# Kernel tuning notes

Hardware: AMD Instinct MI355X
Metric: run time of the kernel (lower is better)

Reference implementation:

```python
import jax, jax.numpy as jnp
import numpy as np

D_MODEL = 512
B, S = 4, 2048


def setup_inputs() -> dict:
    key = jax.random.key(0)
    ks = jax.random.split(key, 12)
    d = D_MODEL
    scale = 1.0 / np.sqrt(d)
    inp = {
        "query": jax.random.normal(ks[0], (B, S, d), dtype=jnp.float32),
        "key":   jax.random.normal(ks[1], (B, S, d), dtype=jnp.float32),
        "value": jax.random.normal(ks[2], (B, S, d), dtype=jnp.float32),
        "mask":  jax.random.uniform(ks[3], (B, S)) < 0.9,
        "num_heads": 8,
        "Wq": jax.random.normal(ks[4], (d, d), dtype=jnp.float32) * scale,
        "bq": jnp.zeros((d,), dtype=jnp.float32),
        "Wk": jax.random.normal(ks[5], (d, d), dtype=jnp.float32) * scale,
        "bk": jnp.zeros((d,), dtype=jnp.float32),
        "Wv": jax.random.normal(ks[6], (d, d), dtype=jnp.float32) * scale,
        "bv": jnp.zeros((d,), dtype=jnp.float32),
        "Wo": jax.random.normal(ks[7], (d, d), dtype=jnp.float32) * scale,
        "bo": jnp.zeros((d,), dtype=jnp.float32),
    }
    return inp


def _mha(query, key, value, mask, num_heads, Wq, bq, Wk, bk, Wv, bv, Wo, bo):
    b, s, d = query.shape
    h = num_heads
    dk = d // h
    # torch Linear: x @ W.T + b ; then split heads -> (b, h, s, dk)
    def proj(x, W, bias):
        return (x @ W.T + bias).reshape(b, s, h, dk).transpose(0, 2, 1, 3)
    q = proj(query, Wq, bq)
    k = proj(key, Wk, bk)
    v = proj(value, Wv, bv)
    scores = jnp.einsum('bhqd,bhkd->bhqk', q, k) / jnp.sqrt(jnp.float32(dk))
    # mask (b, s) broadcast over heads and query positions
    scores = jnp.where(mask[:, None, None, :], scores, -jnp.inf)
    attn = jax.nn.softmax(scores, axis=-1)
    # NaN fix: fully-masked rows produce NaN -> 0 (dropout is identity at eval)
    attn = jnp.where(jnp.isnan(attn), 0.0, attn)
    out = jnp.einsum('bhqk,bhkd->bhqd', attn, v)
    out = out.transpose(0, 2, 1, 3).reshape(b, s, d)
    output = out @ Wo.T + bo
    return output, attn.mean(axis=1)


def reference(query, key, value, mask, num_heads, Wq, bq, Wk, bk, Wv, bv, Wo, bo):
    return _mha(query, key, value, mask, num_heads, Wq, bq, Wk, bk, Wv, bv, Wo, bo)
```

## Files before the change

### kernel.cpp

```cpp
#include <hip/hip_runtime.h>
#include <cstdint>
#include <cstddef>

#define S_LEN 2048
#define D_MODEL 512
#define NHEAD 8
#define DKH 64
#define M_ROWS 8192

typedef unsigned short u16;
typedef unsigned int u32;
typedef short bf16x8 __attribute__((ext_vector_type(8)));
typedef float f32x4 __attribute__((ext_vector_type(4)));

#define MFMA16(a, b, c) __builtin_amdgcn_mfma_f32_16x16x32_bf16((a), (b), (c), 0, 0, 0)

__device__ __forceinline__ u16 f2bf(float f) {
  unsigned u = __float_as_uint(f);
  u += 0x7fffu + ((u >> 16) & 1u);
  return (u16)(u >> 16);
}
__device__ __forceinline__ u32 pack2bf(float f0, float f1) {
  return ((u32)f2bf(f1) << 16) | (u32)f2bf(f0);
}
__device__ __forceinline__ bf16x8 pack8(float4 a, float4 b) {
  union { u32 u[4]; bf16x8 v; } x;
  x.u[0] = pack2bf(a.x, a.y); x.u[1] = pack2bf(a.z, a.w);
  x.u[2] = pack2bf(b.x, b.y); x.u[3] = pack2bf(b.z, b.w);
  return x.v;
}

struct CvtArgs {
  const float* src[7];
  u16* dst[7];
  int n8[7];
};
__global__ __launch_bounds__(256) void cvt_bf16(CvtArgs a) {
  const int ai = blockIdx.y;
  const float* __restrict__ s = a.src[ai];
  u16* __restrict__ d = a.dst[ai];
  const int n8 = a.n8[ai];
  for (int i = blockIdx.x * 256 + threadIdx.x; i < n8; i += gridDim.x * 256) {
    const float4 f0 = *(const float4*)&s[i * 8];
    const float4 f1 = *(const float4*)&s[i * 8 + 4];
    *(bf16x8*)&d[i * 8] = pack8(f0, f1);
  }
}

__global__ __launch_bounds__(512, 4) void proj_qkv(
    const u16* __restrict__ Xq, const u16* __restrict__ Xk, const u16* __restrict__ Xv,
    const u16* __restrict__ Wqb, const u16* __restrict__ Wkb, const u16* __restrict__ Wvb,
    const float* __restrict__ bq, const float* __restrict__ bk, const float* __restrict__ bv,
    u16* __restrict__ Qp, u16* __restrict__ Kp, u16* __restrict__ Vt)
{
  __shared__ __align__(16) u16 wlds[64 * 512];
  const int z = blockIdx.z;
  const u16* __restrict__ X = (z == 0) ? Xk : (z == 1) ? Xv : Xq;
  const u16* __restrict__ W = (z == 0) ? Wkb : (z == 1) ? Wvb : Wqb;
  const float* __restrict__ bias = (z == 0) ? bk : (z == 1) ? bv : bq;
  u16* __restrict__ Y = (z == 0) ? Kp : (z == 1) ? Vt : Qp;
  const int mode = (z == 1) ? 1 : 0;

  const int t = threadIdx.x;
  const int w = t >> 6, lane = t & 63, quad = lane >> 4, lq = lane & 15;
  const int n0 = blockIdx.x * 64;
  const int mb = blockIdx.y * 128 + w * 16;
  const int bb = mb >> 11, s0 = mb & 2047;
  const int h = n0 >> 6;

  for (int i = t; i < 4096; i += 512) {
    const int row = i >> 6, ck = i & 63;
    *(uint4*)&wlds[(row * 512 + ck * 8) ^ ((row & 7) << 3)] =
        *(const uint4*)&W[(size_t)(n0 + row) * D_MODEL + ck * 8];
  }

  bf16x8 xf[16];
#pragma unroll
  for (int ks = 0; ks < 16; ++ks)
    xf[ks] = *(const bf16x8*)&X[(size_t)(mb + lq) * D_MODEL + ks * 32 + quad * 8];
  __syncthreads();

#pragma unroll
  for (int nt = 0; nt < 4; ++nt) {
    const int row = nt * 16 + lq;
    f32x4 acc = {0.f, 0.f, 0.f, 0.f};
#pragma unroll
    for (int ks = 0; ks < 16; ++ks) {
      const bf16x8 wf =
          *(const bf16x8*)&wlds[(row * 512 + ks * 32 + quad * 8) ^ ((row & 7) << 3)];
      acc = MFMA16(xf[ks], wf, acc);
    }
    const float bv2 = bias[n0 + nt * 16 + lq];
    if (mode == 0) {
#pragma unroll
      for (int r = 0; r < 4; ++r)
        Y[(((size_t)(bb * NHEAD + h) * S_LEN) + s0 + quad * 4 + r) * DKH + nt * 16 + lq] =
            f2bf(acc[r] + bv2);
    } else {
      uint2 val;
      val.x = pack2bf(acc[0] + bv2, acc[1] + bv2);
      val.y = pack2bf(acc[2] + bv2, acc[3] + bv2);
      *(uint2*)&Y[(((size_t)(bb * NHEAD + h) * DKH) + nt * 16 + lq) * S_LEN + s0 + quad * 4] = val;
    }
  }
}

__global__ __launch_bounds__(512, 4) void attn_core(
    const u16* __restrict__ Qp,
    const u16* __restrict__ Kp, const u16* __restrict__ Vt,
    const int* __restrict__ mask,
    u16* __restrict__ Oh, float* __restrict__ lis)
{
  __shared__ __align__(16) u16 kvb[2][2][4096];
  __shared__ __align__(16) u16 pst[8][16][72];
  __shared__ u32 gmb[64];

  const int t = threadIdx.x;
  const int w = t >> 6, lane = t & 63, quad = lane >> 4, lq = lane & 15;
  const int srow = t >> 3, sblk = t & 7;
  const int bid = ((int)blockIdx.x & 7) * 64 + ((int)blockIdx.x >> 3);
  const int bb = bid >> 7, h = (bid >> 4) & 7, qc = bid & 15;
  const int qw = qc * 128 + w * 16;
  const size_t hB = (size_t)(bb * NHEAD + h) * S_LEN * DKH;
  const int sslot = srow * 64 + (sblk ^ (srow & 7)) * 8;

#pragma unroll
  for (int p = 0; p < 4; ++p) {
    const int kidx = w * 256 + p * 64 + lane;
    const unsigned long long bal = __ballot(mask[bb * S_LEN + kidx] != 0);
    if (lane == 0) {
      gmb[(w * 256 + p * 64) >> 5] = (u32)bal;
      gmb[((w * 256 + p * 64) >> 5) + 1] = (u32)(bal >> 32);
    }
  }

  uint4 rk = *(const uint4*)&Kp[hB + (size_t)srow * DKH + sblk * 8];
  uint4 rv = *(const uint4*)&Vt[hB + (size_t)srow * S_LEN + sblk * 8];

  bf16x8 qf[2];
#pragma unroll
  for (int ks = 0; ks < 2; ++ks)
    qf[ks] = *(const bf16x8*)&Qp[hB + (size_t)(qw + lq) * DKH + ks * 32 + quad * 8];

  *(uint4*)&kvb[0][0][sslot] = rk;
  *(uint4*)&kvb[0][1][sslot] = rv;
  rk = *(const uint4*)&Kp[hB + (size_t)(64 + srow) * DKH + sblk * 8];
  rv = *(const uint4*)&Vt[hB + (size_t)srow * S_LEN + 64 + sblk * 8];
  __syncthreads();

  f32x4 O[4];
#pragma unroll
  for (int dn = 0; dn < 4; ++dn) { f32x4 z = {0.f, 0.f, 0.f, 0.f}; O[dn] = z; }
  float ls[4] = {0.f, 0.f, 0.f, 0.f};
  const int rx = lq & 7;

#pragma unroll 1
  for (int kt = 0; kt < 32; ++kt) {
    const int c = kt & 1;
    if (kt + 1 < 32) {
      *(uint4*)&kvb[c ^ 1][0][sslot] = rk;
      *(uint4*)&kvb[c ^ 1][1][sslot] = rv;
    }
    if (kt + 2 < 32) {
      const int kb2 = (kt + 2) * 64;
      rk = *(const uint4*)&Kp[hB + (size_t)(kb2 + srow) * DKH + sblk * 8];
      rv = *(const uint4*)&Vt[hB + (size_t)srow * S_LEN + kb2 + sblk * 8];
    }
    const int kb = kt * 64;
    f32x4 p4[4];
    __builtin_amdgcn_s_setprio(1);
#pragma unroll
    for (int kn = 0; kn < 4; ++kn) {
      const bf16x8 k0 = *(const bf16x8*)&kvb[c][0][(kn * 16 + lq) * 64 + (quad ^ rx) * 8];
      const bf16x8 k1 = *(const bf16x8*)&kvb[c][0][(kn * 16 + lq) * 64 + ((4 + quad) ^ rx) * 8];
      f32x4 acc = {0.f, 0.f, 0.f, 0.f};
      acc = MFMA16(qf[0], k0, acc);
      acc = MFMA16(qf[1], k1, acc);
      p4[kn] = acc;
    }
    __builtin_amdgcn_s_setprio(0);
#pragma unroll
    for (int kn = 0; kn < 4; ++kn) {
      const int ki = kb + kn * 16 + lq;
      const float g = ((gmb[ki >> 5] >> (ki & 31)) & 1u) ? 1.f : 0.f;
#pragma unroll
      for (int r = 0; r < 4; ++r) {
        const float e = g * __expf(p4[kn][r] * 0.125f);
        ls[r] += e;
        pst[w][quad * 4 + r][kn * 16 + lq] = f2bf(e);
      }
    }
    bf16x8 pf0 = *(const bf16x8*)&pst[w][lq][quad * 8];
    bf16x8 pf1 = *(const bf16x8*)&pst[w][lq][32 + quad * 8];
    __builtin_amdgcn_s_setprio(1);
#pragma unroll
    for (int dn = 0; dn < 4; ++dn) {
      const bf16x8 v0 = *(const bf16x8*)&kvb[c][1][(dn * 16 + lq) * 64 + (quad ^ rx) * 8];
      const bf16x8 v1 = *(const bf16x8*)&kvb[c][1][(dn * 16 + lq) * 64 + ((4 + quad) ^ rx) * 8];
      O[dn] = MFMA16(pf0, v0, O[dn]);
      O[dn] = MFMA16(pf1, v1, O[dn]);
    }
    __builtin_amdgcn_s_setprio(0);
    __syncthreads();
  }

  float li[4];
#pragma unroll
  for (int r = 0; r < 4; ++r) {
    float v = ls[r];
    v += __shfl_xor(v, 1);
    v += __shfl_xor(v, 2);
    v += __shfl_xor(v, 4);
    v += __shfl_xor(v, 8);
    li[r] = (v > 0.f) ? 1.f / v : 0.f;
  }
  if (lq == 0) {
#pragma unroll
    for (int r = 0; r < 4; ++r)
      lis[(size_t)(bb * NHEAD + h) * S_LEN + qw + quad * 4 + r] = li[r];
  }
#pragma unroll
  for (int dn = 0; dn < 4; ++dn)
#pragma unroll
    for (int r = 0; r < 4; ++r)
      Oh[(size_t)(bb * S_LEN + qw + quad * 4 + r) * D_MODEL + h * 64 + dn * 16 + lq] =
          f2bf(O[dn][r] * li[r]);
}

__global__ __launch_bounds__(512, 4) void oproj_mfma(
    const u16* __restrict__ Oh, const u16* __restrict__ Wb,
    const float* __restrict__ bias, float* __restrict__ out)
{
  __shared__ __align__(16) u16 wlds[64 * 512];
  const int t = threadIdx.x;
  const int w = t >> 6, lane = t & 63, quad = lane >> 4, lq = lane & 15;
  const int n0 = blockIdx.x * 64;
  const int mb = blockIdx.y * 128 + w * 16;

  for (int i = t; i < 4096; i += 512) {
    const int row = i >> 6, ck = i & 63;
    *(uint4*)&wlds[(row * 512 + ck * 8) ^ ((row & 7) << 3)] =
        *(const uint4*)&Wb[(size_t)(n0 + row) * D_MODEL + ck * 8];
  }

  bf16x8 xf[16];
#pragma unroll
  for (int ks = 0; ks < 16; ++ks)
    xf[ks] = *(const bf16x8*)&Oh[(size_t)(mb + lq) * D_MODEL + ks * 32 + quad * 8];
  __syncthreads();

#pragma unroll
  for (int nt = 0; nt < 4; ++nt) {
    const int row = nt * 16 + lq;
    f32x4 acc = {0.f, 0.f, 0.f, 0.f};
#pragma unroll
    for (int ks = 0; ks < 16; ++ks) {
      const bf16x8 wf =
          *(const bf16x8*)&wlds[(row * 512 + ks * 32 + quad * 8) ^ ((row & 7) << 3)];
      acc = MFMA16(xf[ks], wf, acc);
    }
    const float bv = bias[n0 + nt * 16 + lq];
#pragma unroll
    for (int r = 0; r < 4; ++r)
      out[(size_t)(mb + quad * 4 + r) * D_MODEL + n0 + nt * 16 + lq] = acc[r] + bv;
  }
}

__global__ __launch_bounds__(512, 4) void attn_mean(
    const u16* __restrict__ Qp, const u16* __restrict__ Kp,
    const float* __restrict__ lis, const int* __restrict__ mask,
    float* __restrict__ out1)
{
  __shared__ __align__(16) u16 qst[8][32][72];
  __shared__ float lfin[8][32];
  __shared__ u32 gmb[64];

  const int t = threadIdx.x;
  const int w = t >> 6, lane = t & 63, quad = lane >> 4, lq = lane & 15;
  const int bid = ((int)blockIdx.x & 7) * 128 + ((int)blockIdx.x >> 3);
  const int bb = bid >> 8;
  const int q0 = ((bid >> 2) & 63) * 32;
  const int kh = bid & 3;
  const size_t bB = (size_t)bb * NHEAD * S_LEN * DKH;

#pragma unroll
  for (int p = 0; p < 4; ++p) {
    const int kidx = w * 256 + p * 64 + lane;
    const unsigned long long bal = __ballot(mask[bb * S_LEN + kidx] != 0);
    if (lane == 0) {
      gmb[(w * 256 + p * 64) >> 5] = (u32)bal;
      gmb[((w * 256 + p * 64) >> 5) + 1] = (u32)(bal >> 32);
    }
  }
  for (int i = t; i < 2048; i += 512) {
    const int h = i >> 8, qrow = (i >> 3) & 31, d8 = i & 7;
    *(uint4*)&qst[h][qrow][d8 * 8] =
        *(const uint4*)&Qp[bB + (size_t)h * S_LEN * DKH + (size_t)(q0 + qrow) * DKH + d8 * 8];
  }
  if (t < 256) {
    const int h = t >> 5, qr = t & 31;
    lfin[h][qr] = lis[(size_t)(bb * NHEAD + h) * S_LEN + q0 + qr];
  }
  __syncthreads();

  const int kb = kh * 512 + w * 64;

  float am[2][4][4];
#pragma unroll
  for (int qt = 0; qt < 2; ++qt)
#pragma unroll
    for (int kn = 0; kn < 4; ++kn)
#pragma unroll
      for (int r = 0; r < 4; ++r) am[qt][kn][r] = 0.f;

#pragma unroll 1
  for (int h = 0; h < 8; ++h) {
    const size_t hB = bB + (size_t)h * S_LEN * DKH;
    bf16x8 kf[8];
#pragma unroll
    for (int kn = 0; kn < 4; ++kn)
#pragma unroll
      for (int ks = 0; ks < 2; ++ks)
        kf[kn * 2 + ks] =
            *(const bf16x8*)&Kp[hB + (size_t)(kb + kn * 16 + lq) * DKH + ks * 32 + quad * 8];
#pragma unroll
    for (int qt = 0; qt < 2; ++qt) {
      const bf16x8 qh0 = *(const bf16x8*)&qst[h][qt * 16 + lq][quad * 8];
      const bf16x8 qh1 = *(const bf16x8*)&qst[h][qt * 16 + lq][32 + quad * 8];
      const float4 li4 = *(const float4*)&lfin[h][qt * 16 + quad * 4];
#pragma unroll
      for (int kn = 0; kn < 4; ++kn) {
        f32x4 acc = {0.f, 0.f, 0.f, 0.f};
        acc = MFMA16(qh0, kf[kn * 2 + 0], acc);
        acc = MFMA16(qh1, kf[kn * 2 + 1], acc);
        am[qt][kn][0] += __expf(acc[0] * 0.125f) * li4.x;
        am[qt][kn][1] += __expf(acc[1] * 0.125f) * li4.y;
        am[qt][kn][2] += __expf(acc[2] * 0.125f) * li4.z;
        am[qt][kn][3] += __expf(acc[3] * 0.125f) * li4.w;
      }
    }
  }

#pragma unroll
  for (int qt = 0; qt < 2; ++qt)
#pragma unroll
    for (int kn = 0; kn < 4; ++kn) {
      const int ki = kb + kn * 16 + lq;
      const float g8 = ((gmb[ki >> 5] >> (ki & 31)) & 1u) ? 0.125f : 0.f;
#pragma unroll
      for (int r = 0; r < 4; ++r)
        out1[((size_t)(bb * S_LEN + q0 + qt * 16 + quad * 4 + r)) * S_LEN + ki] =
            am[qt][kn][r] * g8;
    }
}

__global__ void beacon_kernel(float* out, float val) { out[0] = val; }

extern "C" void kernel_launch(void* const* d_in, const int* in_sizes, int n_in,
                              void* d_out, int out_size, void* d_ws, size_t ws_size,
                              hipStream_t stream) {
  (void)in_sizes; (void)n_in; (void)out_size;
  const float* q  = (const float*)d_in[0];
  const float* k  = (const float*)d_in[1];
  const float* v  = (const float*)d_in[2];
  const int* mask = (const int*)d_in[3];
  const float* Wq = (const float*)d_in[5];
  const float* bq = (const float*)d_in[6];
  const float* Wk = (const float*)d_in[7];
  const float* bk = (const float*)d_in[8];
  const float* Wv = (const float*)d_in[9];
  const float* bv = (const float*)d_in[10];
  const float* Wo = (const float*)d_in[11];
  const float* bo = (const float*)d_in[12];

  float* out0 = (float*)d_out;
  float* out1 = out0 + (size_t)4 * S_LEN * D_MODEL;

  if (ws_size < (19ull << 20)) {
    beacon_kernel<<<1, 1, 0, stream>>>(out0, 100.0f + (float)(ws_size >> 20));
    return;
  }

  char* ws = (char*)d_ws;
  u16* Kp    = (u16*)(ws);
  u16* Vt    = (u16*)(ws + (8ull << 20));
  float* lis = (float*)(ws + (16ull << 20));
  u16* Qp    = (u16*)(ws + (17ull << 20));

  char* o1 = (char*)out1;
  u16* Oh    = (u16*)o1;
  u16* Xq_bf = (u16*)(o1 + (8ull  << 20));
  u16* Xk_bf = (u16*)(o1 + (16ull << 20));
  u16* Xv_bf = (u16*)(o1 + (24ull << 20));
  u16* Wq_bf = (u16*)(o1 + (32ull << 20));
  u16* Wk_bf = Wq_bf + 262144;
  u16* Wv_bf = Wk_bf + 262144;
  u16* Wo_bf = Wv_bf + 262144;

  CvtArgs ca;
  ca.src[0] = q;  ca.dst[0] = Xq_bf; ca.n8[0] = M_ROWS * D_MODEL / 8;
  ca.src[1] = k;  ca.dst[1] = Xk_bf; ca.n8[1] = M_ROWS * D_MODEL / 8;
  ca.src[2] = v;  ca.dst[2] = Xv_bf; ca.n8[2] = M_ROWS * D_MODEL / 8;
  ca.src[3] = Wq; ca.dst[3] = Wq_bf; ca.n8[3] = D_MODEL * D_MODEL / 8;
  ca.src[4] = Wk; ca.dst[4] = Wk_bf; ca.n8[4] = D_MODEL * D_MODEL / 8;
  ca.src[5] = Wv; ca.dst[5] = Wv_bf; ca.n8[5] = D_MODEL * D_MODEL / 8;
  ca.src[6] = Wo; ca.dst[6] = Wo_bf; ca.n8[6] = D_MODEL * D_MODEL / 8;
  cvt_bf16<<<dim3(256, 7), 256, 0, stream>>>(ca);

  proj_qkv<<<dim3(8, 64, 3), 512, 0, stream>>>(
      Xq_bf, Xk_bf, Xv_bf, Wq_bf, Wk_bf, Wv_bf, bq, bk, bv, Qp, Kp, Vt);

  attn_core<<<512, 512, 0, stream>>>(Qp, Kp, Vt, mask, Oh, lis);
  oproj_mfma<<<dim3(8, 64), 512, 0, stream>>>(Oh, Wo_bf, bo, out0);
  attn_mean<<<1024, 512, 0, stream>>>(Qp, Kp, lis, mask, out1);
}
```

Measured before the change: 326.5 us.

## Double-buffer K loads across heads and stage attn-mean output through LDS

In attn_mean, the K fragments for the next head are loaded into a second register buffer while the current head's MFMAs and exps run, so global-load latency overlaps compute. The output is also written to an LDS staging buffer that aliases the Q tile, then stored as float4 rows instead of scattered 4-byte stores. This targets memory latency and uncoalesced writes of the large attention-mean output. The cost is more registers for the second K buffer and extra block barriers.

After: 365.1 us. +11.8%, slower.

```diff
diff --git a/kernel.cpp b/kernel.cpp
--- a/kernel.cpp
+++ b/kernel.cpp
@@ -271,9 +271,11 @@
     const float* __restrict__ lis, const int* __restrict__ mask,
     float* __restrict__ out1)
 {
-  __shared__ __align__(16) u16 qst[8][32][72];
-  __shared__ float lfin[8][32];
-  __shared__ u32 gmb[64];
+  __shared__ __align__(16) char pool[38912];
+  u16 (*qst)[32][72] = (u16(*)[32][72])pool;
+  float (*lfin)[32]  = (float(*)[32])(pool + 36864);
+  u32* gmb           = (u32*)(pool + 37888);
+  float (*stg)[512]  = (float(*)[512])pool;
 
   const int t = threadIdx.x;
   const int w = t >> 6, lane = t & 63, quad = lane >> 4, lq = lane & 15;
@@ -282,6 +284,7 @@
   const int q0 = ((bid >> 2) & 63) * 32;
   const int kh = bid & 3;
   const size_t bB = (size_t)bb * NHEAD * S_LEN * DKH;
+  const int kb = kh * 512 + w * 64;
 
 #pragma unroll
   for (int p = 0; p < 4; ++p) {
@@ -301,10 +304,20 @@
     const int h = t >> 5, qr = t & 31;
     lfin[h][qr] = lis[(size_t)(bb * NHEAD + h) * S_LEN + q0 + qr];
   }
+
+  bf16x8 kA[8], kB[8];
+  auto loadk = [&](bf16x8 (&dst)[8], int h_) {
+    const size_t hB = bB + (size_t)h_ * S_LEN * DKH;
+#pragma unroll
+    for (int kn = 0; kn < 4; ++kn)
+#pragma unroll
+      for (int ks = 0; ks < 2; ++ks)
+        dst[kn * 2 + ks] =
+            *(const bf16x8*)&Kp[hB + (size_t)(kb + kn * 16 + lq) * DKH + ks * 32 + quad * 8];
+  };
+  loadk(kA, 0);
   __syncthreads();
 
-  const int kb = kh * 512 + w * 64;
-
   float am[2][4][4];
 #pragma unroll
   for (int qt = 0; qt < 2; ++qt)
@@ -313,21 +326,12 @@
 #pragma unroll
       for (int r = 0; r < 4; ++r) am[qt][kn][r] = 0.f;
 
-#pragma unroll 1
-  for (int h = 0; h < 8; ++h) {
-    const size_t hB = bB + (size_t)h * S_LEN * DKH;
-    bf16x8 kf[8];
-#pragma unroll
-    for (int kn = 0; kn < 4; ++kn)
-#pragma unroll
-      for (int ks = 0; ks < 2; ++ks)
-        kf[kn * 2 + ks] =
-            *(const bf16x8*)&Kp[hB + (size_t)(kb + kn * 16 + lq) * DKH + ks * 32 + quad * 8];
+  auto hstep = [&](bf16x8 (&kf)[8], int h_) {
 #pragma unroll
     for (int qt = 0; qt < 2; ++qt) {
-      const bf16x8 qh0 = *(const bf16x8*)&qst[h][qt * 16 + lq][quad * 8];
-      const bf16x8 qh1 = *(const bf16x8*)&qst[h][qt * 16 + lq][32 + quad * 8];
-      const float4 li4 = *(const float4*)&lfin[h][qt * 16 + quad * 4];
+      const bf16x8 qh0 = *(const bf16x8*)&qst[h_][qt * 16 + lq][quad * 8];
+      const bf16x8 qh1 = *(const bf16x8*)&qst[h_][qt * 16 + lq][32 + quad * 8];
+      const float4 li4 = *(const float4*)&lfin[h_][qt * 16 + quad * 4];
 #pragma unroll
       for (int kn = 0; kn < 4; ++kn) {
         f32x4 acc = {0.f, 0.f, 0.f, 0.f};
@@ -339,19 +343,41 @@
         am[qt][kn][3] += __expf(acc[3] * 0.125f) * li4.w;
       }
     }
-  }
-
-#pragma unroll
-  for (int qt = 0; qt < 2; ++qt)
+  };
+
+#pragma unroll 1
+  for (int h = 0; h < 8; h += 2) {
+    loadk(kB, h + 1);
+    hstep(kA, h);
+    if (h + 2 < 8) loadk(kA, h + 2);
+    hstep(kB, h + 1);
+  }
+
+  __syncthreads();
+#pragma unroll 1
+  for (int hf = 0; hf < 2; ++hf) {
 #pragma unroll
     for (int kn = 0; kn < 4; ++kn) {
       const int ki = kb + kn * 16 + lq;
+      const int cl = w * 64 + kn * 16 + lq;
       const float g8 = ((gmb[ki >> 5] >> (ki & 31)) & 1u) ? 0.125f : 0.f;
 #pragma unroll
       for (int r = 0; r < 4; ++r)
-        out1[((size_t)(bb * S_LEN + q0 + qt * 16 + quad * 4 + r)) * S_LEN + ki] =
-            am[qt][kn][r] * g8;
-    }
+        stg[quad * 4 + r][cl] = am[hf][kn][r] * g8;
+    }
+    __syncthreads();
+    {
+      const int row = t >> 5, j = t & 31;
+      float* dst = &out1[((size_t)(bb * S_LEN + q0 + hf * 16 + row)) * S_LEN + kh * 512];
+      const float* src = &stg[row][0];
+#pragma unroll
+      for (int it = 0; it < 4; ++it) {
+        const int c4 = (j + it * 32) * 4;
+        *(float4*)&dst[c4] = *(const float4*)&src[c4];
+      }
+    }
+    if (hf == 0) __syncthreads();
+  }
 }
 
 __global__ void beacon_kernel(float* out, float val) { out[0] = val; }
```
